# Optimization experiments

Measured on AMD Instinct MI355X. Metric: run time of the kernel, lower is better.

## Reference

```python
import jax, jax.numpy as jnp
import numpy as np

B, C, H, W = 8, 512, 32, 32
N_HEADS = 4
D_K = C // N_HEADS  # 128


def setup_inputs() -> dict:
    key = jax.random.key(0)
    k1, k2, k3, k4, k5 = jax.random.split(key, 5)
    x = jax.random.normal(k1, (B, C, H, W), dtype=jnp.float32)
    # projection: Linear(in_ch, n_heads*d_k*3)
    Wp = jax.random.normal(k2, (C, N_HEADS * D_K * 3), dtype=jnp.float32) * (C ** -0.5)
    bp = jax.random.normal(k3, (N_HEADS * D_K * 3,), dtype=jnp.float32) * 0.01
    # output: Linear(n_heads*d_k, in_ch)
    Wo = jax.random.normal(k4, (N_HEADS * D_K, C), dtype=jnp.float32) * ((N_HEADS * D_K) ** -0.5)
    bo = jax.random.normal(k5, (C,), dtype=jnp.float32) * 0.01
    return {"x": x, "Wp": Wp, "bp": bp, "Wo": Wo, "bo": bo}


def reference(x, Wp, bp, Wo, bo):
    b, c, h, w = x.shape
    scale = D_K ** -0.5
    # [B, C, H, W] -> [B, N, C], N = H*W
    xs = x.reshape(b, c, h * w).transpose(0, 2, 1)
    qkv = (xs @ Wp + bp).reshape(b, h * w, N_HEADS, 3 * D_K)
    q, k, v = jnp.split(qkv, 3, axis=-1)  # each [B, N, H, D]
    attn = jnp.einsum('bihd,bjhd->bijh', q, k) * scale
    attn = jax.nn.softmax(attn, axis=2)  # softmax over j (keys)
    out = jnp.einsum('bijh,bjhd->bihd', attn, v)
    out = out.reshape(b, h * w, N_HEADS * D_K)
    out = out @ Wo + bo
    out = out + xs  # residual (note: GroupNorm is unused in the original forward)
    return out.transpose(0, 2, 1).reshape(b, c, h, w)
```

## Files before the change

### kernel.cpp

```cpp
#include <hip/hip_runtime.h>

#define NB 8
#define NC 512
#define NTOK 1024
#define NHEADS 4
#define DKH 128

typedef unsigned short u16;
typedef __attribute__((ext_vector_type(8))) short bf16x8;
typedef __attribute__((ext_vector_type(4))) float f32x4;

__device__ inline u16 f2b(float f) {
    union { float f; unsigned u; } v; v.f = f;
    unsigned r = v.u + 0x7fffu + ((v.u >> 16) & 1u);
    return (u16)(r >> 16);
}

__device__ __forceinline__ void gll16(const u16* g, u16* l) {
    __builtin_amdgcn_global_load_lds((const __attribute__((address_space(1))) unsigned*)g,
                                     (__attribute__((address_space(3))) unsigned*)l, 16, 0, 0);
}

__global__ __launch_bounds__(256) void prep(const float* __restrict__ x, const float* __restrict__ Wp,
                                            const float* __restrict__ Wo,
                                            u16* __restrict__ xsb, u16* __restrict__ WpT, u16* __restrict__ WoT)
{
    __shared__ float tile[32][33];
    const int z = blockIdx.z;
    const float* src; u16* dst; int R, Cc;
    if (z == 0)      { src = Wp; dst = WpT; R = 512; Cc = 1536; }
    else if (z == 1) { if (blockIdx.x >= 16) return; src = Wo; dst = WoT; R = 512; Cc = 512; }
    else             { if (blockIdx.x >= 32) return;
                       src = x + (long)(z-2)*NC*NTOK; dst = xsb + (long)(z-2)*NTOK*NC; R = NC; Cc = NTOK; }
    int c0 = blockIdx.x * 32, r0 = blockIdx.y * 32;
    int tx = threadIdx.x, ty = threadIdx.y;
    #pragma unroll
    for (int k = 0; k < 4; ++k)
        tile[ty + 8*k][tx] = src[(long)(r0 + ty + 8*k) * Cc + c0 + tx];
    __syncthreads();
    #pragma unroll
    for (int k = 0; k < 4; ++k)
        dst[(long)(c0 + ty + 8*k) * R + r0 + tx] = f2b(tile[tx][ty + 8*k]);
}

__global__ __launch_bounds__(512, 2) void gemm_qkv(const u16* __restrict__ WpT, const u16* __restrict__ xsb,
                                                   const float* __restrict__ bp,
                                                   u16* __restrict__ qg, u16* __restrict__ kg, u16* __restrict__ vg)
{
    __shared__ union SmU {
        struct { u16 As[2][256][64]; u16 Bs[2][256][64]; } s;
        u16 Os[8][64][72];
    } sm;
    const int tid = threadIdx.x;
    const int raw = blockIdx.x;
    const int L = (raw & 7) * 24 + (raw >> 3);
    const int mb = L % 6, nb = L / 6;
    const int m0 = mb * 256;
    const int n0 = nb * 256;
    const int w = tid >> 6, lane = tid & 63, quad = lane >> 4, lc = lane & 15;
    const int mo = (w & 1) * 128, no = (w >> 1) * 64;
    const int sw8 = (((lane & 7) ^ (lane >> 3)) << 3);
    const int xs = lc & 15 & 7;
    const int srow = (lane >> 3);

    f32x4 acc[8][4] = {};

    #pragma unroll
    for (int p = 0; p < 4; ++p) {
        int row = w*32 + p*8 + srow;
        gll16(&WpT[(long)(m0 + row) * NC + 0 + sw8], &sm.s.As[0][w*32 + p*8][0]);
        gll16(&xsb[(long)(n0 + row) * NC + 0 + sw8], &sm.s.Bs[0][w*32 + p*8][0]);
    }

    for (int t = 0; t < 8; ++t) {
        if (t < 7) {
            const long kk = (long)(t + 1) * 64;
            const int nbuf = (t + 1) & 1;
            #pragma unroll
            for (int p = 0; p < 4; ++p) {
                int row = w*32 + p*8 + srow;
                gll16(&WpT[(long)(m0 + row) * NC + kk + sw8], &sm.s.As[nbuf][w*32 + p*8][0]);
                gll16(&xsb[(long)(n0 + row) * NC + kk + sw8], &sm.s.Bs[nbuf][w*32 + p*8][0]);
            }
            asm volatile("s_waitcnt vmcnt(8)" ::: "memory");
        } else {
            asm volatile("s_waitcnt vmcnt(0)" ::: "memory");
        }
        __builtin_amdgcn_s_barrier();
        __builtin_amdgcn_sched_barrier(0);

        const int cb = t & 1;
        #pragma unroll
        for (int ks = 0; ks < 2; ++ks) {
            bf16x8 af[8], bfr[4];
            #pragma unroll
            for (int mt = 0; mt < 8; ++mt)
                af[mt] = *(const bf16x8*)&sm.s.As[cb][mo + mt*16 + lc][((ks*4 + quad) ^ xs) << 3];
            #pragma unroll
            for (int nt = 0; nt < 4; ++nt)
                bfr[nt] = *(const bf16x8*)&sm.s.Bs[cb][no + nt*16 + lc][((ks*4 + quad) ^ xs) << 3];
            __builtin_amdgcn_s_setprio(1);
            #pragma unroll
            for (int mt = 0; mt < 8; ++mt)
                #pragma unroll
                for (int nt = 0; nt < 4; ++nt)
                    acc[mt][nt] = __builtin_amdgcn_mfma_f32_16x16x32_bf16(af[mt], bfr[nt], acc[mt][nt], 0, 0, 0);
            __builtin_amdgcn_s_setprio(0);
        }
        __builtin_amdgcn_s_barrier();
    }

    const int bb = n0 >> 10;
    const int nblk = n0 & 1023;
    const int pb = (m0 + mo) >> 7;
    const int h = pb / 3;
    const int sel = pb % 3;
    const long bhbase = (long)(bb * NHEADS + h);

    #pragma unroll
    for (int mh = 0; mh < 2; ++mh) {
        const int d0 = mh * 64;
        #pragma unroll
        for (int mt4 = 0; mt4 < 4; ++mt4) {
            int mt = mh*4 + mt4;
            int cq0 = m0 + mo + mt*16 + quad*4;
            float b0 = bp[cq0+0], b1 = bp[cq0+1], b2 = bp[cq0+2], b3 = bp[cq0+3];
            #pragma unroll
            for (int nt = 0; nt < 4; ++nt) {
                f32x4 a = acc[mt][nt];
                int nl = nt*16 + lc;
                int ml = mt4*16 + quad*4;
                u16 e0 = f2b(a[0]+b0), e1 = f2b(a[1]+b1), e2 = f2b(a[2]+b2), e3 = f2b(a[3]+b3);
                if (sel == 2) {
                    sm.Os[w][ml+0][nl] = e0; sm.Os[w][ml+1][nl] = e1;
                    sm.Os[w][ml+2][nl] = e2; sm.Os[w][ml+3][nl] = e3;
                } else {
                    sm.Os[w][nl][ml+0] = e0; sm.Os[w][nl][ml+1] = e1;
                    sm.Os[w][nl][ml+2] = e2; sm.Os[w][nl][ml+3] = e3;
                }
            }
        }
        __builtin_amdgcn_sched_barrier(0);

        if (sel == 2) {
            #pragma unroll
            for (int pass = 0; pass < 8; ++pass) {
                int ml  = pass*8 + srow;
                int nl0 = (lane & 7) * 8;
                bf16x8 vv = *(const bf16x8*)&sm.Os[w][ml][nl0];
                *(bf16x8*)&vg[((bhbase*DKH + d0 + ml) << 10) + nblk + no + sw8] = vv;
            }
        } else if (sel == 1) {
            #pragma unroll
            for (int pass = 0; pass < 8; ++pass) {
                int nl  = pass*8 + srow;
                int ml0 = (lane & 7) * 8;
                bf16x8 vv = *(const bf16x8*)&sm.Os[w][nl][ml0];
                *(bf16x8*)&kg[((bhbase*NTOK + nblk + no + nl) << 7) + d0 + sw8] = vv;
            }
        } else {
            #pragma unroll
            for (int pass = 0; pass < 8; ++pass) {
                int nl  = pass*8 + srow;
                int ml0 = (lane & 7) * 8;
                bf16x8 vv = *(const bf16x8*)&sm.Os[w][nl][ml0];
                *(bf16x8*)&qg[((bhbase*NTOK + nblk + no + nl) << 7) + d0 + ml0] = vv;
            }
        }
        __builtin_amdgcn_sched_barrier(0);
    }
}

__global__ __launch_bounds__(512) void attn(const u16* __restrict__ qg, const u16* __restrict__ kg,
                                            const u16* __restrict__ vtg, u16* __restrict__ ho)
{
    __shared__ u16 Ks[2][64*128];
    __shared__ u16 Vt[2][128*64];
    __shared__ u16 Ps[8][16][72];
    const int tid = threadIdx.x;
    const int w = tid >> 6, lane = tid & 63, quad = lane >> 4, lc = lane & 15;
    const int id = blockIdx.x;
    const int xcd = id & 7, rest = id >> 3, sub = rest & 3, bx = rest >> 2;
    const int pr = xcd + sub*8;
    const int b = pr >> 2, h = pr & 3;
    const int i0 = bx*128 + w*16;
    const long bh = (long)(b * NHEADS + h) << 17;
    const u16* qb = qg + bh;
    const u16* kb = kg + bh;
    const u16* vb = vtg + bh;
    const float SL2E = 0.08838834764831845f * 1.4426950408889634f;

    bf16x8 qf[4];
    #pragma unroll
    for (int ks = 0; ks < 4; ++ks)
        qf[ks] = *(const bf16x8*)&qb[(long)(i0 + lc) * DKH + ks*32 + quad*8];

    f32x4 o[8] = {};
    float lsum = 0.f;
    const int xs = lc & 7;

    #pragma unroll
    for (int p = 0; p < 2; ++p) {
        int ck = (w*2 + p)*64 + lane;
        gll16(&kb[(long)ck * 8], &Ks[0][(w*2 + p)*512]);
        gll16(&vb[(((long)(ck >> 3)) << 10) + (ck & 7)*8], &Vt[0][(w*2 + p)*512]);
    }

    for (int t = 0; t < 16; ++t) {
        __syncthreads();
        if (t < 15) {
            long jo = (long)(t+1) * 64;
            #pragma unroll
            for (int p = 0; p < 2; ++p) {
                int ck = (w*2 + p)*64 + lane;
                gll16(&kb[jo*128 + (long)ck*8], &Ks[(t+1)&1][(w*2 + p)*512]);
                gll16(&vb[(((long)(ck >> 3)) << 10) + jo + (ck & 7)*8], &Vt[(t+1)&1][(w*2 + p)*512]);
            }
        }
        const u16* K = Ks[t&1];
        const u16* V = Vt[t&1];

        f32x4 s[4] = {};
        #pragma unroll
        for (int ks = 0; ks < 4; ++ks)
            #pragma unroll
            for (int jt = 0; jt < 4; ++jt) {
                bf16x8 kf = *(const bf16x8*)&K[(jt*16 + lc)*128 + (((ks*4 + quad) ^ xs) << 3)];
                s[jt] = __builtin_amdgcn_mfma_f32_16x16x32_bf16(kf, qf[ks], s[jt], 0, 0, 0);
            }

        #pragma unroll
        for (int jt = 0; jt < 4; ++jt) {
            float p0 = __builtin_amdgcn_exp2f(s[jt][0] * SL2E);
            float p1 = __builtin_amdgcn_exp2f(s[jt][1] * SL2E);
            float p2 = __builtin_amdgcn_exp2f(s[jt][2] * SL2E);
            float p3 = __builtin_amdgcn_exp2f(s[jt][3] * SL2E);
            lsum += (p0 + p1) + (p2 + p3);
            ushort4 pk;
            pk.x = f2b(p0); pk.y = f2b(p1); pk.z = f2b(p2); pk.w = f2b(p3);
            *(ushort4*)&Ps[w][lc][jt*16 + quad*4] = pk;
        }
        __builtin_amdgcn_sched_barrier(0);

        #pragma unroll
        for (int ks2 = 0; ks2 < 2; ++ks2) {
            bf16x8 pf = *(const bf16x8*)&Ps[w][lc][ks2*32 + quad*8];
            #pragma unroll
            for (int dt = 0; dt < 8; ++dt) {
                bf16x8 vf = *(const bf16x8*)&V[(dt*16 + lc)*64 + (((ks2*4 + quad) ^ xs) << 3)];
                o[dt] = __builtin_amdgcn_mfma_f32_16x16x32_bf16(vf, pf, o[dt], 0, 0, 0);
            }
        }
    }

    lsum += __shfl_xor(lsum, 16);
    lsum += __shfl_xor(lsum, 32);
    float inv = 1.0f / lsum;

    #pragma unroll
    for (int dt = 0; dt < 8; ++dt) {
        ushort4 pk;
        pk.x = f2b(o[dt][0] * inv); pk.y = f2b(o[dt][1] * inv);
        pk.z = f2b(o[dt][2] * inv); pk.w = f2b(o[dt][3] * inv);
        *(ushort4*)&ho[(long)(b*NTOK + i0 + lc) * NC + h*DKH + dt*16 + quad*4] = pk;
    }
}

__global__ __launch_bounds__(256) void gemm_out(const u16* __restrict__ WoT, const u16* __restrict__ ho,
                                                const float* __restrict__ bo, const float* __restrict__ xin,
                                                float* __restrict__ dout)
{
    __shared__ struct { u16 As[128][64]; u16 Bs[64][64]; } sm;
    const int tid = threadIdx.x;
    const int m0 = blockIdx.x * 128;
    const int n0 = blockIdx.y * 64;
    const int w = tid >> 6, lane = tid & 63, quad = lane >> 4, lc = lane & 15;
    const int mo = (w & 1) * 64, no = (w >> 1) * 32;
    const int sw8 = (((lane & 7) ^ (lane >> 3)) << 3);
    const int xs = lc & 7;

    f32x4 acc[4][2] = {};

    for (int k0 = 0; k0 < NC; k0 += 64) {
        __syncthreads();
        #pragma unroll
        for (int p = 0; p < 4; ++p) {
            int row = w*32 + p*8 + (lane >> 3);
            gll16(&WoT[(long)(m0 + row) * NC + k0 + sw8], &sm.As[w*32 + p*8][0]);
        }
        #pragma unroll
        for (int p = 0; p < 2; ++p) {
            int row = w*16 + p*8 + (lane >> 3);
            gll16(&ho[(long)(n0 + row) * NC + k0 + sw8], &sm.Bs[w*16 + p*8][0]);
        }
        __syncthreads();
        #pragma unroll
        for (int ks = 0; ks < 2; ++ks) {
            bf16x8 af[4], bfr[2];
            #pragma unroll
            for (int t = 0; t < 4; ++t)
                af[t] = *(const bf16x8*)&sm.As[mo + t*16 + lc][((ks*4 + quad) ^ xs) << 3];
            #pragma unroll
            for (int t = 0; t < 2; ++t)
                bfr[t] = *(const bf16x8*)&sm.Bs[no + t*16 + lc][((ks*4 + quad) ^ xs) << 3];
            #pragma unroll
            for (int mt = 0; mt < 4; ++mt)
                #pragma unroll
                for (int nt = 0; nt < 2; ++nt)
                    acc[mt][nt] = __builtin_amdgcn_mfma_f32_16x16x32_bf16(af[mt], bfr[nt], acc[mt][nt], 0, 0, 0);
        }
    }

    const int bb = n0 >> 10;
    #pragma unroll
    for (int mt = 0; mt < 4; ++mt) {
        int cc0 = m0 + mo + mt*16 + quad*4;
        float b0 = bo[cc0+0], b1 = bo[cc0+1], b2 = bo[cc0+2], b3 = bo[cc0+3];
        #pragma unroll
        for (int nt = 0; nt < 2; ++nt) {
            int nl = (n0 + no + nt*16 + lc) & (NTOK - 1);
            f32x4 a = acc[mt][nt];
            long ix = ((long)(bb*NC + cc0) << 10) + nl;
            dout[ix]             = a[0] + b0 + xin[ix];
            dout[ix + (1 << 10)] = a[1] + b1 + xin[ix + (1 << 10)];
            dout[ix + (2 << 10)] = a[2] + b2 + xin[ix + (2 << 10)];
            dout[ix + (3 << 10)] = a[3] + b3 + xin[ix + (3 << 10)];
        }
    }
}

extern "C" void kernel_launch(void* const* d_in, const int* in_sizes, int n_in,
                              void* d_out, int out_size, void* d_ws, size_t ws_size,
                              hipStream_t stream)
{
    (void)in_sizes; (void)n_in; (void)out_size; (void)ws_size;
    const float* x  = (const float*)d_in[0];
    const float* Wp = (const float*)d_in[1];
    const float* bp = (const float*)d_in[2];
    const float* Wo = (const float*)d_in[3];
    const float* bo = (const float*)d_in[4];
    float* out = (float*)d_out;

    u16* ws  = (u16*)d_ws;
    u16* xsb = ws;
    u16* WpT = xsb + (long)NB * NTOK * NC;
    u16* WoT = WpT + 1536L * 512;
    u16* qg  = WoT + 512L * 512;
    u16* kg  = qg + (long)NB * NHEADS * NTOK * DKH;
    u16* vtg = kg + (long)NB * NHEADS * NTOK * DKH;
    u16* ho  = vtg + (long)NB * NHEADS * NTOK * DKH;

    prep<<<dim3(48, 16, 10), dim3(32, 8), 0, stream>>>(x, Wp, Wo, xsb, WpT, WoT);
    gemm_qkv<<<dim3(192), 512, 0, stream>>>(WpT, xsb, bp, qg, kg, vtg);
    attn<<<dim3(256), 512, 0, stream>>>(qg, kg, vtg, ho);
    gemm_out<<<dim3(NC/128, (NB*NTOK)/64), 256, 0, stream>>>(WoT, ho, bo, x, out);
}
```

Baseline: 141.5 us.

## Split attention key range across warp pairs with 32-row query tiles per warp

Each warp in the attention kernel now handles 32 query rows and half of every 64-key tile, instead of 16 rows over all keys. Each K and V fragment read from LDS feeds two MFMAs, which roughly halves LDS fragment traffic per MFMA. The two key halves produce partial O sums and row sums, and these are merged through a shared-memory union in the epilogue. This adds two block barriers, extra LDS for the reduction, and more accumulator registers (two sets of 8 f32x4), which could lower occupancy.

Result: slower. 257.3 us (+81.8%).

```diff
diff --git a/kernel.cpp b/kernel.cpp
--- a/kernel.cpp
+++ b/kernel.cpp
@@ -60,7 +60,7 @@
     const int w = tid >> 6, lane = tid & 63, quad = lane >> 4, lc = lane & 15;
     const int mo = (w & 1) * 128, no = (w >> 1) * 64;
     const int sw8 = (((lane & 7) ^ (lane >> 3)) << 3);
-    const int xs = lc & 15 & 7;
+    const int xs = lc & 7;
     const int srow = (lane >> 3);
 
     f32x4 acc[8][4] = {};
@@ -174,36 +174,40 @@
 __global__ __launch_bounds__(512) void attn(const u16* __restrict__ qg, const u16* __restrict__ kg,
                                             const u16* __restrict__ vtg, u16* __restrict__ ho)
 {
-    __shared__ u16 Ks[2][64*128];
-    __shared__ u16 Vt[2][128*64];
-    __shared__ u16 Ps[8][16][72];
+    __shared__ union {
+        struct { u16 Ks[2][64*128]; u16 Vt[2][128*64]; u16 Ps[8][32][40]; } m;
+        struct { float Om[4][2][32][68]; float Lm[2][4][32]; } g;
+    } sm;
     const int tid = threadIdx.x;
     const int w = tid >> 6, lane = tid & 63, quad = lane >> 4, lc = lane & 15;
+    const int iw = w & 3, jw = w >> 2;
     const int id = blockIdx.x;
     const int xcd = id & 7, rest = id >> 3, sub = rest & 3, bx = rest >> 2;
     const int pr = xcd + sub*8;
     const int b = pr >> 2, h = pr & 3;
-    const int i0 = bx*128 + w*16;
+    const int i0 = bx*128 + iw*32;
     const long bh = (long)(b * NHEADS + h) << 17;
     const u16* qb = qg + bh;
     const u16* kb = kg + bh;
     const u16* vb = vtg + bh;
     const float SL2E = 0.08838834764831845f * 1.4426950408889634f;
 
-    bf16x8 qf[4];
-    #pragma unroll
-    for (int ks = 0; ks < 4; ++ks)
-        qf[ks] = *(const bf16x8*)&qb[(long)(i0 + lc) * DKH + ks*32 + quad*8];
-
-    f32x4 o[8] = {};
-    float lsum = 0.f;
+    bf16x8 qf[2][4];
+    #pragma unroll
+    for (int it = 0; it < 2; ++it)
+        #pragma unroll
+        for (int ks = 0; ks < 4; ++ks)
+            qf[it][ks] = *(const bf16x8*)&qb[(long)(i0 + it*16 + lc) * DKH + ks*32 + quad*8];
+
+    f32x4 o[2][8] = {};
+    float lsum[2] = {0.f, 0.f};
     const int xs = lc & 7;
 
     #pragma unroll
     for (int p = 0; p < 2; ++p) {
         int ck = (w*2 + p)*64 + lane;
-        gll16(&kb[(long)ck * 8], &Ks[0][(w*2 + p)*512]);
-        gll16(&vb[(((long)(ck >> 3)) << 10) + (ck & 7)*8], &Vt[0][(w*2 + p)*512]);
+        gll16(&kb[(long)ck * 8], &sm.m.Ks[0][(w*2 + p)*512]);
+        gll16(&vb[(((long)(ck >> 3)) << 10) + (ck & 7)*8], &sm.m.Vt[0][(w*2 + p)*512]);
     }
 
     for (int t = 0; t < 16; ++t) {
@@ -213,56 +217,80 @@
             #pragma unroll
             for (int p = 0; p < 2; ++p) {
                 int ck = (w*2 + p)*64 + lane;
-                gll16(&kb[jo*128 + (long)ck*8], &Ks[(t+1)&1][(w*2 + p)*512]);
-                gll16(&vb[(((long)(ck >> 3)) << 10) + jo + (ck & 7)*8], &Vt[(t+1)&1][(w*2 + p)*512]);
-            }
-        }
-        const u16* K = Ks[t&1];
-        const u16* V = Vt[t&1];
-
-        f32x4 s[4] = {};
+                gll16(&kb[jo*128 + (long)ck*8], &sm.m.Ks[(t+1)&1][(w*2 + p)*512]);
+                gll16(&vb[(((long)(ck >> 3)) << 10) + jo + (ck & 7)*8], &sm.m.Vt[(t+1)&1][(w*2 + p)*512]);
+            }
+        }
+        const u16* K = sm.m.Ks[t&1];
+        const u16* V = sm.m.Vt[t&1];
+
+        f32x4 s[2][2] = {};
         #pragma unroll
         for (int ks = 0; ks < 4; ++ks)
             #pragma unroll
-            for (int jt = 0; jt < 4; ++jt) {
-                bf16x8 kf = *(const bf16x8*)&K[(jt*16 + lc)*128 + (((ks*4 + quad) ^ xs) << 3)];
-                s[jt] = __builtin_amdgcn_mfma_f32_16x16x32_bf16(kf, qf[ks], s[jt], 0, 0, 0);
-            }
-
-        #pragma unroll
-        for (int jt = 0; jt < 4; ++jt) {
-            float p0 = __builtin_amdgcn_exp2f(s[jt][0] * SL2E);
-            float p1 = __builtin_amdgcn_exp2f(s[jt][1] * SL2E);
-            float p2 = __builtin_amdgcn_exp2f(s[jt][2] * SL2E);
-            float p3 = __builtin_amdgcn_exp2f(s[jt][3] * SL2E);
-            lsum += (p0 + p1) + (p2 + p3);
+            for (int jt = 0; jt < 2; ++jt) {
+                bf16x8 kf = *(const bf16x8*)&K[(jw*32 + jt*16 + lc)*128 + (((ks*4 + quad) ^ xs) << 3)];
+                s[0][jt] = __builtin_amdgcn_mfma_f32_16x16x32_bf16(kf, qf[0][ks], s[0][jt], 0, 0, 0);
+                s[1][jt] = __builtin_amdgcn_mfma_f32_16x16x32_bf16(kf, qf[1][ks], s[1][jt], 0, 0, 0);
+            }
+
+        #pragma unroll
+        for (int it = 0; it < 2; ++it)
+            #pragma unroll
+            for (int jt = 0; jt < 2; ++jt) {
+                float p0 = __builtin_amdgcn_exp2f(s[it][jt][0] * SL2E);
+                float p1 = __builtin_amdgcn_exp2f(s[it][jt][1] * SL2E);
+                float p2 = __builtin_amdgcn_exp2f(s[it][jt][2] * SL2E);
+                float p3 = __builtin_amdgcn_exp2f(s[it][jt][3] * SL2E);
+                lsum[it] += (p0 + p1) + (p2 + p3);
+                ushort4 pk;
+                pk.x = f2b(p0); pk.y = f2b(p1); pk.z = f2b(p2); pk.w = f2b(p3);
+                *(ushort4*)&sm.m.Ps[w][it*16 + lc][jt*16 + quad*4] = pk;
+            }
+        __builtin_amdgcn_sched_barrier(0);
+
+        bf16x8 pf0 = *(const bf16x8*)&sm.m.Ps[w][lc]     [quad*8];
+        bf16x8 pf1 = *(const bf16x8*)&sm.m.Ps[w][16 + lc][quad*8];
+        #pragma unroll
+        for (int dt = 0; dt < 8; ++dt) {
+            bf16x8 vf = *(const bf16x8*)&V[(dt*16 + lc)*64 + (((jw*4 + quad) ^ xs) << 3)];
+            o[0][dt] = __builtin_amdgcn_mfma_f32_16x16x32_bf16(vf, pf0, o[0][dt], 0, 0, 0);
+            o[1][dt] = __builtin_amdgcn_mfma_f32_16x16x32_bf16(vf, pf1, o[1][dt], 0, 0, 0);
+        }
+    }
+
+    #pragma unroll
+    for (int it = 0; it < 2; ++it) {
+        lsum[it] += __shfl_xor(lsum[it], 16);
+        lsum[it] += __shfl_xor(lsum[it], 32);
+    }
+
+    __syncthreads();
+    #pragma unroll
+    for (int it = 0; it < 2; ++it) {
+        #pragma unroll
+        for (int d4 = 0; d4 < 4; ++d4) {
+            int dt = (1 - jw)*4 + d4;
+            *(f32x4*)&sm.g.Om[iw][1 - jw][it*16 + lc][d4*16 + quad*4] = o[it][dt];
+        }
+        if (quad == 0) sm.g.Lm[jw][iw][it*16 + lc] = lsum[it];
+    }
+    __syncthreads();
+    #pragma unroll
+    for (int it = 0; it < 2; ++it) {
+        float lt = lsum[it] + sm.g.Lm[1 - jw][iw][it*16 + lc];
+        float inv = 1.0f / lt;
+        long rowbase = (long)(b*NTOK + i0 + it*16 + lc) * NC + h*DKH + jw*64;
+        #pragma unroll
+        for (int d4 = 0; d4 < 4; ++d4) {
+            int dt = jw*4 + d4;
+            f32x4 part = *(const f32x4*)&sm.g.Om[iw][jw][it*16 + lc][d4*16 + quad*4];
+            f32x4 tot = o[it][dt] + part;
             ushort4 pk;
-            pk.x = f2b(p0); pk.y = f2b(p1); pk.z = f2b(p2); pk.w = f2b(p3);
-            *(ushort4*)&Ps[w][lc][jt*16 + quad*4] = pk;
-        }
-        __builtin_amdgcn_sched_barrier(0);
-
-        #pragma unroll
-        for (int ks2 = 0; ks2 < 2; ++ks2) {
-            bf16x8 pf = *(const bf16x8*)&Ps[w][lc][ks2*32 + quad*8];
-            #pragma unroll
-            for (int dt = 0; dt < 8; ++dt) {
-                bf16x8 vf = *(const bf16x8*)&V[(dt*16 + lc)*64 + (((ks2*4 + quad) ^ xs) << 3)];
-                o[dt] = __builtin_amdgcn_mfma_f32_16x16x32_bf16(vf, pf, o[dt], 0, 0, 0);
-            }
-        }
-    }
-
-    lsum += __shfl_xor(lsum, 16);
-    lsum += __shfl_xor(lsum, 32);
-    float inv = 1.0f / lsum;
-
-    #pragma unroll
-    for (int dt = 0; dt < 8; ++dt) {
-        ushort4 pk;
-        pk.x = f2b(o[dt][0] * inv); pk.y = f2b(o[dt][1] * inv);
-        pk.z = f2b(o[dt][2] * inv); pk.w = f2b(o[dt][3] * inv);
-        *(ushort4*)&ho[(long)(b*NTOK + i0 + lc) * NC + h*DKH + dt*16 + quad*4] = pk;
+            pk.x = f2b(tot[0] * inv); pk.y = f2b(tot[1] * inv);
+            pk.z = f2b(tot[2] * inv); pk.w = f2b(tot[3] * inv);
+            *(ushort4*)&ho[rowbase + d4*16 + quad*4] = pk;
+        }
     }
 }
 
```

## Process two query tiles per warp in attention to reuse K/V fragments

Applied to the files above, without the earlier changes.

Each warp in the attention kernel now handles 32 query rows (two 16-row tiles) instead of 16, so every K and V fragment read from LDS feeds two MFMAs. The grid is halved from 256 to 128 blocks and the P buffer doubles. This cuts LDS traffic and global K/V reloads per query. The cost is more registers and fewer blocks, which on a chip with 256 CUs leaves half the CUs idle during attention.

Measured after the change: 154.1 us. 8.9% more time.

```diff
diff --git a/kernel.cpp b/kernel.cpp
--- a/kernel.cpp
+++ b/kernel.cpp
@@ -60,7 +60,7 @@
     const int w = tid >> 6, lane = tid & 63, quad = lane >> 4, lc = lane & 15;
     const int mo = (w & 1) * 128, no = (w >> 1) * 64;
     const int sw8 = (((lane & 7) ^ (lane >> 3)) << 3);
-    const int xs = lc & 15 & 7;
+    const int xs = lc & 7;
     const int srow = (lane >> 3);
 
     f32x4 acc[8][4] = {};
@@ -176,27 +176,29 @@
 {
     __shared__ u16 Ks[2][64*128];
     __shared__ u16 Vt[2][128*64];
-    __shared__ u16 Ps[8][16][72];
+    __shared__ u16 Ps[8][32][72];
     const int tid = threadIdx.x;
     const int w = tid >> 6, lane = tid & 63, quad = lane >> 4, lc = lane & 15;
     const int id = blockIdx.x;
     const int xcd = id & 7, rest = id >> 3, sub = rest & 3, bx = rest >> 2;
     const int pr = xcd + sub*8;
     const int b = pr >> 2, h = pr & 3;
-    const int i0 = bx*128 + w*16;
+    const int i0 = bx*256 + w*32;
     const long bh = (long)(b * NHEADS + h) << 17;
     const u16* qb = qg + bh;
     const u16* kb = kg + bh;
     const u16* vb = vtg + bh;
     const float SL2E = 0.08838834764831845f * 1.4426950408889634f;
 
-    bf16x8 qf[4];
-    #pragma unroll
-    for (int ks = 0; ks < 4; ++ks)
-        qf[ks] = *(const bf16x8*)&qb[(long)(i0 + lc) * DKH + ks*32 + quad*8];
-
-    f32x4 o[8] = {};
-    float lsum = 0.f;
+    bf16x8 qf[2][4];
+    #pragma unroll
+    for (int it = 0; it < 2; ++it)
+        #pragma unroll
+        for (int ks = 0; ks < 4; ++ks)
+            qf[it][ks] = *(const bf16x8*)&qb[(long)(i0 + it*16 + lc) * DKH + ks*32 + quad*8];
+
+    f32x4 o[2][8] = {};
+    float lsum0 = 0.f, lsum1 = 0.f;
     const int xs = lc & 7;
 
     #pragma unroll
@@ -220,49 +222,62 @@
         const u16* K = Ks[t&1];
         const u16* V = Vt[t&1];
 
-        f32x4 s[4] = {};
+        f32x4 s[2][4] = {};
         #pragma unroll
         for (int ks = 0; ks < 4; ++ks)
             #pragma unroll
             for (int jt = 0; jt < 4; ++jt) {
                 bf16x8 kf = *(const bf16x8*)&K[(jt*16 + lc)*128 + (((ks*4 + quad) ^ xs) << 3)];
-                s[jt] = __builtin_amdgcn_mfma_f32_16x16x32_bf16(kf, qf[ks], s[jt], 0, 0, 0);
-            }
-
-        #pragma unroll
-        for (int jt = 0; jt < 4; ++jt) {
-            float p0 = __builtin_amdgcn_exp2f(s[jt][0] * SL2E);
-            float p1 = __builtin_amdgcn_exp2f(s[jt][1] * SL2E);
-            float p2 = __builtin_amdgcn_exp2f(s[jt][2] * SL2E);
-            float p3 = __builtin_amdgcn_exp2f(s[jt][3] * SL2E);
-            lsum += (p0 + p1) + (p2 + p3);
-            ushort4 pk;
-            pk.x = f2b(p0); pk.y = f2b(p1); pk.z = f2b(p2); pk.w = f2b(p3);
-            *(ushort4*)&Ps[w][lc][jt*16 + quad*4] = pk;
-        }
+                s[0][jt] = __builtin_amdgcn_mfma_f32_16x16x32_bf16(kf, qf[0][ks], s[0][jt], 0, 0, 0);
+                s[1][jt] = __builtin_amdgcn_mfma_f32_16x16x32_bf16(kf, qf[1][ks], s[1][jt], 0, 0, 0);
+            }
+
+        #pragma unroll
+        for (int it = 0; it < 2; ++it)
+            #pragma unroll
+            for (int jt = 0; jt < 4; ++jt) {
+                float p0 = __builtin_amdgcn_exp2f(s[it][jt][0] * SL2E);
+                float p1 = __builtin_amdgcn_exp2f(s[it][jt][1] * SL2E);
+                float p2 = __builtin_amdgcn_exp2f(s[it][jt][2] * SL2E);
+                float p3 = __builtin_amdgcn_exp2f(s[it][jt][3] * SL2E);
+                if (it == 0) lsum0 += (p0 + p1) + (p2 + p3);
+                else         lsum1 += (p0 + p1) + (p2 + p3);
+                ushort4 pk;
+                pk.x = f2b(p0); pk.y = f2b(p1); pk.z = f2b(p2); pk.w = f2b(p3);
+                *(ushort4*)&Ps[w][it*16 + lc][jt*16 + quad*4] = pk;
+            }
         __builtin_amdgcn_sched_barrier(0);
 
         #pragma unroll
         for (int ks2 = 0; ks2 < 2; ++ks2) {
-            bf16x8 pf = *(const bf16x8*)&Ps[w][lc][ks2*32 + quad*8];
+            bf16x8 pf0 = *(const bf16x8*)&Ps[w][lc]     [ks2*32 + quad*8];
+            bf16x8 pf1 = *(const bf16x8*)&Ps[w][16 + lc][ks2*32 + quad*8];
             #pragma unroll
             for (int dt = 0; dt < 8; ++dt) {
                 bf16x8 vf = *(const bf16x8*)&V[(dt*16 + lc)*64 + (((ks2*4 + quad) ^ xs) << 3)];
-                o[dt] = __builtin_amdgcn_mfma_f32_16x16x32_bf16(vf, pf, o[dt], 0, 0, 0);
-            }
-        }
-    }
-
-    lsum += __shfl_xor(lsum, 16);
-    lsum += __shfl_xor(lsum, 32);
-    float inv = 1.0f / lsum;
+                o[0][dt] = __builtin_amdgcn_mfma_f32_16x16x32_bf16(vf, pf0, o[0][dt], 0, 0, 0);
+                o[1][dt] = __builtin_amdgcn_mfma_f32_16x16x32_bf16(vf, pf1, o[1][dt], 0, 0, 0);
+            }
+        }
+    }
+
+    lsum0 += __shfl_xor(lsum0, 16);
+    lsum0 += __shfl_xor(lsum0, 32);
+    lsum1 += __shfl_xor(lsum1, 16);
+    lsum1 += __shfl_xor(lsum1, 32);
+    float inv0 = 1.0f / lsum0;
+    float inv1 = 1.0f / lsum1;
 
     #pragma unroll
     for (int dt = 0; dt < 8; ++dt) {
         ushort4 pk;
-        pk.x = f2b(o[dt][0] * inv); pk.y = f2b(o[dt][1] * inv);
-        pk.z = f2b(o[dt][2] * inv); pk.w = f2b(o[dt][3] * inv);
+        pk.x = f2b(o[0][dt][0] * inv0); pk.y = f2b(o[0][dt][1] * inv0);
+        pk.z = f2b(o[0][dt][2] * inv0); pk.w = f2b(o[0][dt][3] * inv0);
         *(ushort4*)&ho[(long)(b*NTOK + i0 + lc) * NC + h*DKH + dt*16 + quad*4] = pk;
+        ushort4 pk1;
+        pk1.x = f2b(o[1][dt][0] * inv1); pk1.y = f2b(o[1][dt][1] * inv1);
+        pk1.z = f2b(o[1][dt][2] * inv1); pk1.w = f2b(o[1][dt][3] * inv1);
+        *(ushort4*)&ho[(long)(b*NTOK + i0 + 16 + lc) * NC + h*DKH + dt*16 + quad*4] = pk1;
     }
 }
 
@@ -352,6 +367,6 @@
 
     prep<<<dim3(48, 16, 10), dim3(32, 8), 0, stream>>>(x, Wp, Wo, xsb, WpT, WoT);
     gemm_qkv<<<dim3(192), 512, 0, stream>>>(WpT, xsb, bp, qg, kg, vtg);
-    attn<<<dim3(256), 512, 0, stream>>>(qg, kg, vtg, ho);
+    attn<<<dim3(128), 512, 0, stream>>>(qg, kg, vtg, ho);
     gemm_out<<<dim3(NC/128, (NB*NTOK)/64), 256, 0, stream>>>(WoT, ho, bo, x, out);
 }
```

## Triple-buffer K/V tiles in attention with prefetch distance two and partial vmcnt waits

Applied to the files above, without the earlier changes.

The attention kernel moves from double to triple buffering of K and V tiles in LDS and issues the global-to-LDS loads two iterations ahead. A partial vmcnt wait replaces the full __syncthreads drain, so loads for the next tile can stay in flight while the current tile is computed. LDS use grows by one K and one V buffer, about 32 KB, which may lower occupancy. A redundant mask in gemm_qkv is also simplified.

Result: no change. 142.3 us (+0.5%).

```diff
diff --git a/kernel.cpp b/kernel.cpp
--- a/kernel.cpp
+++ b/kernel.cpp
@@ -60,7 +60,7 @@
     const int w = tid >> 6, lane = tid & 63, quad = lane >> 4, lc = lane & 15;
     const int mo = (w & 1) * 128, no = (w >> 1) * 64;
     const int sw8 = (((lane & 7) ^ (lane >> 3)) << 3);
-    const int xs = lc & 15 & 7;
+    const int xs = lc & 7;
     const int srow = (lane >> 3);
 
     f32x4 acc[8][4] = {};
@@ -174,8 +174,8 @@
 __global__ __launch_bounds__(512) void attn(const u16* __restrict__ qg, const u16* __restrict__ kg,
                                             const u16* __restrict__ vtg, u16* __restrict__ ho)
 {
-    __shared__ u16 Ks[2][64*128];
-    __shared__ u16 Vt[2][128*64];
+    __shared__ u16 Ks[3][64*128];
+    __shared__ u16 Vt[3][128*64];
     __shared__ u16 Ps[8][16][72];
     const int tid = threadIdx.x;
     const int w = tid >> 6, lane = tid & 63, quad = lane >> 4, lc = lane & 15;
@@ -194,31 +194,41 @@
     #pragma unroll
     for (int ks = 0; ks < 4; ++ks)
         qf[ks] = *(const bf16x8*)&qb[(long)(i0 + lc) * DKH + ks*32 + quad*8];
+    __builtin_amdgcn_sched_barrier(0);
 
     f32x4 o[8] = {};
     float lsum = 0.f;
     const int xs = lc & 7;
 
     #pragma unroll
-    for (int p = 0; p < 2; ++p) {
-        int ck = (w*2 + p)*64 + lane;
-        gll16(&kb[(long)ck * 8], &Ks[0][(w*2 + p)*512]);
-        gll16(&vb[(((long)(ck >> 3)) << 10) + (ck & 7)*8], &Vt[0][(w*2 + p)*512]);
-    }
-
+    for (int tt = 0; tt < 2; ++tt) {
+        long jo = (long)tt * 64;
+        #pragma unroll
+        for (int p = 0; p < 2; ++p) {
+            int ck = (w*2 + p)*64 + lane;
+            gll16(&kb[jo*128 + (long)ck*8], &Ks[tt][(w*2 + p)*512]);
+            gll16(&vb[(((long)(ck >> 3)) << 10) + jo + (ck & 7)*8], &Vt[tt][(w*2 + p)*512]);
+        }
+    }
+
+    int cur = 0, nxt2 = 2;
     for (int t = 0; t < 16; ++t) {
-        __syncthreads();
-        if (t < 15) {
-            long jo = (long)(t+1) * 64;
+        if (t < 15) { asm volatile("s_waitcnt vmcnt(4)" ::: "memory"); }
+        else        { asm volatile("s_waitcnt vmcnt(0)" ::: "memory"); }
+        __builtin_amdgcn_s_barrier();
+        __builtin_amdgcn_sched_barrier(0);
+
+        if (t + 2 < 16) {
+            long jo = (long)(t + 2) * 64;
             #pragma unroll
             for (int p = 0; p < 2; ++p) {
                 int ck = (w*2 + p)*64 + lane;
-                gll16(&kb[jo*128 + (long)ck*8], &Ks[(t+1)&1][(w*2 + p)*512]);
-                gll16(&vb[(((long)(ck >> 3)) << 10) + jo + (ck & 7)*8], &Vt[(t+1)&1][(w*2 + p)*512]);
-            }
-        }
-        const u16* K = Ks[t&1];
-        const u16* V = Vt[t&1];
+                gll16(&kb[jo*128 + (long)ck*8], &Ks[nxt2][(w*2 + p)*512]);
+                gll16(&vb[(((long)(ck >> 3)) << 10) + jo + (ck & 7)*8], &Vt[nxt2][(w*2 + p)*512]);
+            }
+        }
+        const u16* K = Ks[cur];
+        const u16* V = Vt[cur];
 
         f32x4 s[4] = {};
         #pragma unroll
@@ -251,6 +261,9 @@
                 o[dt] = __builtin_amdgcn_mfma_f32_16x16x32_bf16(vf, pf, o[dt], 0, 0, 0);
             }
         }
+
+        cur  = (cur  == 2) ? 0 : cur + 1;
+        nxt2 = (nxt2 == 2) ? 0 : nxt2 + 1;
     }
 
     lsum += __shfl_xor(lsum, 16);
```
